# Optimization experiments

Measured on AMD Instinct MI355X. Metric: run time of the kernel, lower is better.

## Reference

```python
import jax, jax.numpy as jnp
import numpy as np

AUDIO_DIM, TEXT_DIM, HIDDEN_DIM = 512, 768, 512
B, AUDIO_LEN, TEXT_LEN = 8, 2048, 512


def setup_inputs() -> dict:
    key = jax.random.key(0)
    ks = jax.random.split(key, 9)
    audio_features = jax.random.normal(ks[0], (B, AUDIO_LEN, AUDIO_DIM), dtype=jnp.float32)
    text_features = jax.random.normal(ks[1], (B, TEXT_LEN, TEXT_DIM), dtype=jnp.float32)
    text_mask = jax.random.randint(ks[2], (B, TEXT_LEN), 0, 2).astype(jnp.int32)
    # Linear params (PyTorch default init scale ~ U(-1/sqrt(fan_in), 1/sqrt(fan_in)))
    def lin(kw, kb, fan_in, fan_out):
        bound = 1.0 / np.sqrt(fan_in)
        W = jax.random.uniform(kw, (fan_in, fan_out), minval=-bound, maxval=bound, dtype=jnp.float32)
        b = jax.random.uniform(kb, (fan_out,), minval=-bound, maxval=bound, dtype=jnp.float32)
        return W, b
    Wq, bq = lin(ks[3], ks[4], AUDIO_DIM, HIDDEN_DIM)
    Wk, bk = lin(ks[5], ks[6], TEXT_DIM, HIDDEN_DIM)
    Wv, bv = lin(ks[7], ks[8], TEXT_DIM, HIDDEN_DIM)
    return {
        "audio_features": audio_features,
        "text_features": text_features,
        "Wq": Wq, "bq": bq, "Wk": Wk, "bk": bk, "Wv": Wv, "bv": bv,
        "text_mask": text_mask,
    }


def reference(audio_features, text_features, Wq, bq, Wk, bk, Wv, bv, text_mask):
    scale = HIDDEN_DIM ** -0.5
    q = jnp.einsum("bad,dh->bah", audio_features, Wq) + bq  # (B, A, H)
    k = jnp.einsum("btd,dh->bth", text_features, Wk) + bk   # (B, T, H)
    v = jnp.einsum("btd,dh->bth", text_features, Wv) + bv   # (B, T, H)
    scores = jnp.einsum("bah,bth->bat", q, k) * scale        # (B, A, T)
    mask = text_mask[:, None, :]  # (B, 1, T)
    scores = jnp.where(mask == 0, -jnp.inf, scores)
    attn = jax.nn.softmax(scores, axis=-1)
    # dropout is identity in eval mode
    enhanced_audio = jnp.einsum("bat,bth->bah", attn, v)     # (B, A, H)
    return enhanced_audio
```

## Files before the change

kernel.cpp:

```cpp
#include <hip/hip_runtime.h>
#include <cstdint>
#include <cstddef>

#define AUDIO_DIM 512
#define TEXT_DIM  768
#define HIDDEN    512
#define BATCH     8
#define ALEN      2048
#define TLEN      512

typedef _Float16 half8 __attribute__((ext_vector_type(8)));
typedef _Float16 half4_t __attribute__((ext_vector_type(4)));
typedef float floatx4 __attribute__((ext_vector_type(4)));

#define AS1 __attribute__((address_space(1)))
#define AS3 __attribute__((address_space(3)))

__device__ __forceinline__ void gload_lds16(const void* g, void* l) {
    __builtin_amdgcn_global_load_lds((const AS1 void*)g, (AS3 void*)l, 16, 0, 0);
}

__device__ __forceinline__ int swz(int r) { return (r >> 1) & 3; }

__global__ __launch_bounds__(256) void prep(
    const float* __restrict__ audio, const float* __restrict__ text,
    const float* __restrict__ Wq, const float* __restrict__ Wk,
    const float* __restrict__ Wv,
    _Float16* __restrict__ audio_h, _Float16* __restrict__ text_h,
    _Float16* __restrict__ Wq_t, _Float16* __restrict__ Wk_t,
    _Float16* __restrict__ Wv_t)
{
    __shared__ _Float16 tt[32 * 33];
    const int bid = blockIdx.x, tid = threadIdx.x;
    if (bid < 11264) {
        const float* src; _Float16* dst; int i;
        if (bid < 8192) { src = audio; dst = audio_h; i = bid * 256 + tid; }
        else            { src = text;  dst = text_h;  i = (bid - 8192) * 256 + tid; }
        float4 v = ((const float4*)src)[i];
        half4_t h;
        h.x = (_Float16)v.x; h.y = (_Float16)v.y; h.z = (_Float16)v.z; h.w = (_Float16)v.w;
        ((half4_t*)dst)[i] = h;
    } else {
        const float* src; _Float16* dst; int R, lb;
        if (bid < 11520)      { lb = bid - 11264; src = Wq; dst = Wq_t; R = 512; }
        else if (bid < 11904) { lb = bid - 11520; src = Wk; dst = Wk_t; R = 768; }
        else                  { lb = bid - 11904; src = Wv; dst = Wv_t; R = 768; }
        const int C = 512;
        const int c0 = (lb & 15) * 32, r0 = (lb >> 4) * 32;
        const int tx = tid & 31, ty = tid >> 5;
#pragma unroll
        for (int i = 0; i < 4; i++) {
            int r = ty + i * 8;
            tt[r * 33 + tx] = (_Float16)src[(size_t)(r0 + r) * C + c0 + tx];
        }
        __syncthreads();
#pragma unroll
        for (int i = 0; i < 4; i++) {
            int r = ty + i * 8;
            dst[(size_t)(c0 + r) * R + r0 + tx] = tt[tx * 33 + r];
        }
    }
}

template <bool OUT16, bool ROWBIAS>
__device__ __forceinline__ void gemm_body(
    const _Float16* __restrict__ A, const _Float16* __restrict__ Bt,
    const float* __restrict__ bias, void* __restrict__ Cp,
    int N, int K, int m0, int n0, _Float16* Asm, _Float16* Bsm)
{
    const int tid = threadIdx.x;
    const int l = tid & 63, w = tid >> 6;
    const int wm = w >> 1, wn = w & 1;
    const int srow = l >> 2, sj = l & 3;
    const int q = l >> 4, c16 = l & 15;

    floatx4 acc[4][4] = {};

    for (int k0 = 0; k0 < K; k0 += 32) {
        if (k0) __syncthreads();
#pragma unroll
        for (int i = 0; i < 2; i++) {
            int rb = (w * 2 + i) * 16;
            int r = rb + srow;
            int cc = sj ^ swz(r);
            gload_lds16(A + (size_t)(m0 + r) * K + k0 + cc * 8, Asm + rb * 32);
            gload_lds16(Bt + (size_t)(n0 + r) * K + k0 + cc * 8, Bsm + rb * 32);
        }
        __syncthreads();

        half8 af[4], bf[4];
#pragma unroll
        for (int t = 0; t < 4; t++) {
            int rA = wm * 64 + t * 16 + c16;
            af[t] = *(const half8*)&Asm[rA * 32 + ((q ^ swz(rA)) << 3)];
            int rB = wn * 64 + t * 16 + c16;
            bf[t] = *(const half8*)&Bsm[rB * 32 + ((q ^ swz(rB)) << 3)];
        }
#pragma unroll
        for (int mi = 0; mi < 4; mi++)
#pragma unroll
            for (int ni = 0; ni < 4; ni++)
                acc[mi][ni] = __builtin_amdgcn_mfma_f32_16x16x32_f16(
                    af[mi], bf[ni], acc[mi][ni], 0, 0, 0);
    }

    if (OUT16) {
        float bcol[4];
        float brow[4][4];
        if (!ROWBIAS) {
#pragma unroll
            for (int ni = 0; ni < 4; ni++)
                bcol[ni] = bias[n0 + wn * 64 + ni * 16 + c16];
        } else {
#pragma unroll
            for (int mi = 0; mi < 4; mi++) {
                float4 b4 = *(const float4*)&bias[m0 + wm * 64 + mi * 16 + q * 4];
                brow[mi][0] = b4.x; brow[mi][1] = b4.y;
                brow[mi][2] = b4.z; brow[mi][3] = b4.w;
            }
        }
        _Float16* C = (_Float16*)Cp;
#pragma unroll
        for (int ni = 0; ni < 4; ni++) {
            int col = n0 + wn * 64 + ni * 16 + c16;
#pragma unroll
            for (int mi = 0; mi < 4; mi++) {
                int row = m0 + wm * 64 + mi * 16 + q * 4;
#pragma unroll
                for (int r = 0; r < 4; r++) {
                    float b = ROWBIAS ? brow[mi][r] : bcol[ni];
                    C[(size_t)(row + r) * N + col] = (_Float16)(acc[mi][ni][r] + b);
                }
            }
        }
    } else {
        float* C = (float*)Cp;
#pragma unroll
        for (int ni = 0; ni < 4; ni++) {
            int col = n0 + wn * 64 + ni * 16 + c16;
#pragma unroll
            for (int mi = 0; mi < 4; mi++) {
                int row = m0 + wm * 64 + mi * 16 + q * 4;
#pragma unroll
                for (int r = 0; r < 4; r++)
                    C[(size_t)(row + r) * N + col] = acc[mi][ni][r];
            }
        }
    }
}

__global__ __launch_bounds__(256, 2) void qkv_gemm(
    const _Float16* __restrict__ audio_h, const _Float16* __restrict__ text_h,
    const _Float16* __restrict__ Wq_t, const _Float16* __restrict__ Wk_t,
    const _Float16* __restrict__ Wv_t,
    const float* __restrict__ bq, const float* __restrict__ bk,
    const float* __restrict__ bv,
    _Float16* __restrict__ Qh, _Float16* __restrict__ Kh,
    _Float16* __restrict__ Vt)
{
    __shared__ __align__(16) _Float16 Asm[128 * 32];
    __shared__ __align__(16) _Float16 Bsm[128 * 32];
    const int bid = blockIdx.x;
    if (bid < 512) {
        gemm_body<true, false>(audio_h, Wq_t, bq, Qh, 512, 512,
                               (bid >> 2) * 128, (bid & 3) * 128, Asm, Bsm);
    } else if (bid < 640) {
        int lb = bid - 512;
        gemm_body<true, false>(text_h, Wk_t, bk, Kh, 512, 768,
                               (lb >> 2) * 128, (lb & 3) * 128, Asm, Bsm);
    } else {
        int lb = bid - 640;
        int z = lb >> 4, by = (lb >> 2) & 3, bx = lb & 3;
        gemm_body<true, true>(Wv_t, text_h + (size_t)z * 393216, bv,
                              Vt + (size_t)z * 262144, 512, 768,
                              by * 128, bx * 128, Asm, Bsm);
    }
}

#define QT 32
#define PSTR 544

__global__ __launch_bounds__(256, 2) void attn_fused(
    const _Float16* __restrict__ Qh, const _Float16* __restrict__ Kh,
    const _Float16* __restrict__ Vt, const int* __restrict__ mask,
    float* __restrict__ out)
{
    __shared__ __align__(16) _Float16 Qs[QT * 32];
    __shared__ __align__(16) _Float16 KV[512 * 32];
    __shared__ __align__(16) _Float16 Pl[QT * PSTR];
    __shared__ float red[4][QT];
    __shared__ float red2[4][QT];
    const int tid = threadIdx.x, l = tid & 63, w = tid >> 6;
    const int b = blockIdx.y, a0 = blockIdx.x * QT;
    const _Float16* Qb = Qh + (size_t)(b * ALEN + a0) * HIDDEN;
    const _Float16* Kb = Kh + (size_t)b * TLEN * HIDDEN;
    const _Float16* Vb = Vt + (size_t)b * HIDDEN * TLEN;
    const int srow = l >> 2, sj = l & 3;
    const int q = l >> 4, c16 = l & 15;

    floatx4 acc[2][8] = {};
    for (int k0 = 0; k0 < HIDDEN; k0 += 32) {
        if (k0) __syncthreads();
        if (w < 2) {
            int rb = w * 16;
            int r = rb + srow;
            int cc = sj ^ swz(r);
            gload_lds16(Qb + (size_t)r * HIDDEN + k0 + cc * 8, Qs + rb * 32);
        }
#pragma unroll
        for (int i = 0; i < 8; i++) {
            int rb = (w * 8 + i) * 16;
            int r = rb + srow;
            int cc = sj ^ swz(r);
            gload_lds16(Kb + (size_t)r * HIDDEN + k0 + cc * 8, KV + rb * 32);
        }
        __syncthreads();

        half8 af[2], bf[8];
#pragma unroll
        for (int t = 0; t < 2; t++) {
            int rA = t * 16 + c16;
            af[t] = *(const half8*)&Qs[rA * 32 + ((q ^ swz(rA)) << 3)];
        }
#pragma unroll
        for (int t = 0; t < 8; t++) {
            int rB = w * 128 + t * 16 + c16;
            bf[t] = *(const half8*)&KV[rB * 32 + ((q ^ swz(rB)) << 3)];
        }
#pragma unroll
        for (int mi = 0; mi < 2; mi++)
#pragma unroll
            for (int ni = 0; ni < 8; ni++)
                acc[mi][ni] = __builtin_amdgcn_mfma_f32_16x16x32_f16(
                    af[mi], bf[ni], acc[mi][ni], 0, 0, 0);
    }

    const float scale = 0.044194173824159216f;
    int mv[8];
#pragma unroll
    for (int ni = 0; ni < 8; ni++)
        mv[ni] = mask[b * TLEN + w * 128 + ni * 16 + c16];
#pragma unroll
    for (int mi = 0; mi < 2; mi++)
#pragma unroll
        for (int ni = 0; ni < 8; ni++)
#pragma unroll
            for (int r = 0; r < 4; r++)
                acc[mi][ni][r] = mv[ni] ? acc[mi][ni][r] * scale : -1e30f;

    float mx[2][4];
#pragma unroll
    for (int mi = 0; mi < 2; mi++)
#pragma unroll
        for (int r = 0; r < 4; r++) {
            float m = -1e30f;
#pragma unroll
            for (int ni = 0; ni < 8; ni++) m = fmaxf(m, acc[mi][ni][r]);
#pragma unroll
            for (int off = 1; off <= 8; off <<= 1) m = fmaxf(m, __shfl_xor(m, off));
            mx[mi][r] = m;
        }
    if (c16 == 0)
#pragma unroll
        for (int mi = 0; mi < 2; mi++)
#pragma unroll
            for (int r = 0; r < 4; r++) red[w][mi * 16 + q * 4 + r] = mx[mi][r];
    __syncthreads();
#pragma unroll
    for (int mi = 0; mi < 2; mi++)
#pragma unroll
        for (int r = 0; r < 4; r++) {
            int row = mi * 16 + q * 4 + r;
            mx[mi][r] = fmaxf(fmaxf(red[0][row], red[1][row]),
                              fmaxf(red[2][row], red[3][row]));
        }

    float sm[2][4];
#pragma unroll
    for (int mi = 0; mi < 2; mi++)
#pragma unroll
        for (int r = 0; r < 4; r++) {
            float s = 0.f;
#pragma unroll
            for (int ni = 0; ni < 8; ni++) {
                float e = __expf(acc[mi][ni][r] - mx[mi][r]);
                acc[mi][ni][r] = e;
                s += e;
            }
#pragma unroll
            for (int off = 1; off <= 8; off <<= 1) s += __shfl_xor(s, off);
            sm[mi][r] = s;
        }
    if (c16 == 0)
#pragma unroll
        for (int mi = 0; mi < 2; mi++)
#pragma unroll
            for (int r = 0; r < 4; r++) red2[w][mi * 16 + q * 4 + r] = sm[mi][r];
    __syncthreads();

#pragma unroll
    for (int mi = 0; mi < 2; mi++)
#pragma unroll
        for (int r = 0; r < 4; r++) {
            int row = mi * 16 + q * 4 + r;
            float inv = 1.f / (red2[0][row] + red2[1][row] + red2[2][row] + red2[3][row]);
#pragma unroll
            for (int ni = 0; ni < 8; ni++) {
                int t = w * 128 + ni * 16 + c16;
                int chunk = t >> 3;
                int chunkS = (chunk & ~3) | ((chunk & 3) ^ ((row >> 1) & 3));
                Pl[row * PSTR + chunkS * 8 + (t & 7)] = (_Float16)(acc[mi][ni][r] * inv);
            }
        }
    __syncthreads();

    floatx4 oacc[2][8] = {};
    for (int k0 = 0; k0 < TLEN; k0 += 32) {
        if (k0) __syncthreads();
#pragma unroll
        for (int i = 0; i < 8; i++) {
            int rb = (w * 8 + i) * 16;
            int r = rb + srow;
            int cc = sj ^ swz(r);
            gload_lds16(Vb + (size_t)r * TLEN + k0 + cc * 8, KV + rb * 32);
        }
        __syncthreads();

        half8 pf[2], vf[8];
#pragma unroll
        for (int mi = 0; mi < 2; mi++) {
            int row = mi * 16 + c16;
            int chunkS = (k0 >> 3) + (q ^ ((c16 >> 1) & 3));
            pf[mi] = *(const half8*)&Pl[row * PSTR + chunkS * 8];
        }
#pragma unroll
        for (int t = 0; t < 8; t++) {
            int rB = w * 128 + t * 16 + c16;
            vf[t] = *(const half8*)&KV[rB * 32 + ((q ^ swz(rB)) << 3)];
        }
#pragma unroll
        for (int mi = 0; mi < 2; mi++)
#pragma unroll
            for (int ni = 0; ni < 8; ni++)
                oacc[mi][ni] = __builtin_amdgcn_mfma_f32_16x16x32_f16(
                    pf[mi], vf[ni], oacc[mi][ni], 0, 0, 0);
    }

#pragma unroll
    for (int ni = 0; ni < 8; ni++) {
        int col = w * 128 + ni * 16 + c16;
#pragma unroll
        for (int mi = 0; mi < 2; mi++) {
            int row = mi * 16 + q * 4;
#pragma unroll
            for (int r = 0; r < 4; r++)
                out[(size_t)(b * ALEN + a0 + row + r) * HIDDEN + col] =
                    oacc[mi][ni][r];
        }
    }
}

extern "C" void kernel_launch(void* const* d_in, const int* in_sizes, int n_in,
                              void* d_out, int out_size, void* d_ws, size_t ws_size,
                              hipStream_t stream)
{
    const float* audio = (const float*)d_in[0];
    const float* text  = (const float*)d_in[1];
    const float* Wq    = (const float*)d_in[2];
    const float* bq    = (const float*)d_in[3];
    const float* Wk    = (const float*)d_in[4];
    const float* bk    = (const float*)d_in[5];
    const float* Wv    = (const float*)d_in[6];
    const float* bv    = (const float*)d_in[7];
    const int*   maskp = (const int*)d_in[8];
    float* out = (float*)d_out;

    _Float16* audio_h = (_Float16*)d_out;

    _Float16* ws16   = (_Float16*)d_ws;
    _Float16* text_h = ws16;
    _Float16* Wq_t   = text_h + 3145728;
    _Float16* Wk_t   = Wq_t + 262144;
    _Float16* Wv_t   = Wk_t + 393216;
    _Float16* Kh     = Wv_t + 393216;
    _Float16* Vt     = Kh + 2097152;
    _Float16* Qh     = Vt + 2097152;

    prep<<<12288, 256, 0, stream>>>(audio, text, Wq, Wk, Wv,
                                    audio_h, text_h, Wq_t, Wk_t, Wv_t);
    qkv_gemm<<<768, 256, 0, stream>>>(audio_h, text_h, Wq_t, Wk_t, Wv_t,
                                      bq, bk, bv, Qh, Kh, Vt);
    attn_fused<<<dim3(ALEN / QT, BATCH), 256, 0, stream>>>(Qh, Kh, Vt, maskp, out);
}
```

Baseline: 177.8 us.

## Load Q/K/V MFMA fragments directly from global memory, drop LDS staging

The attention kernel now reads Q, K and V operand fragments straight from global memory into registers rather than staging them through shared memory with global_load_lds and barriers. This removes the per-iteration __syncthreads and frees the Qs/KV LDS buffers, and the launch bound is raised to 4 blocks per CU for more occupancy. In exchange each wave issues strided 16-byte global loads, and there is no longer any sharing of K/V tiles within a block, so the design leans on L1/L2 caching. The higher occupancy target may also cause register spills given the large accumulator arrays.

Result: slower. 222.9 us (+25.4%).

```diff
diff --git a/kernel.cpp b/kernel.cpp
--- a/kernel.cpp
+++ b/kernel.cpp
@@ -180,13 +180,11 @@
 #define QT 32
 #define PSTR 544
 
-__global__ __launch_bounds__(256, 2) void attn_fused(
+__global__ __launch_bounds__(256, 4) void attn_fused(
     const _Float16* __restrict__ Qh, const _Float16* __restrict__ Kh,
     const _Float16* __restrict__ Vt, const int* __restrict__ mask,
     float* __restrict__ out)
 {
-    __shared__ __align__(16) _Float16 Qs[QT * 32];
-    __shared__ __align__(16) _Float16 KV[512 * 32];
     __shared__ __align__(16) _Float16 Pl[QT * PSTR];
     __shared__ float red[4][QT];
     __shared__ float red2[4][QT];
@@ -195,38 +193,27 @@
     const _Float16* Qb = Qh + (size_t)(b * ALEN + a0) * HIDDEN;
     const _Float16* Kb = Kh + (size_t)b * TLEN * HIDDEN;
     const _Float16* Vb = Vt + (size_t)b * HIDDEN * TLEN;
-    const int srow = l >> 2, sj = l & 3;
     const int q = l >> 4, c16 = l & 15;
 
+    const _Float16* arow[2];
+#pragma unroll
+    for (int mi = 0; mi < 2; mi++)
+        arow[mi] = Qb + (size_t)(mi * 16 + c16) * HIDDEN + q * 8;
+    const _Float16* brow[8];
+#pragma unroll
+    for (int ni = 0; ni < 8; ni++)
+        brow[ni] = Kb + (size_t)(w * 128 + ni * 16 + c16) * HIDDEN + q * 8;
+
     floatx4 acc[2][8] = {};
+#pragma unroll 4
     for (int k0 = 0; k0 < HIDDEN; k0 += 32) {
-        if (k0) __syncthreads();
-        if (w < 2) {
-            int rb = w * 16;
-            int r = rb + srow;
-            int cc = sj ^ swz(r);
-            gload_lds16(Qb + (size_t)r * HIDDEN + k0 + cc * 8, Qs + rb * 32);
-        }
-#pragma unroll
-        for (int i = 0; i < 8; i++) {
-            int rb = (w * 8 + i) * 16;
-            int r = rb + srow;
-            int cc = sj ^ swz(r);
-            gload_lds16(Kb + (size_t)r * HIDDEN + k0 + cc * 8, KV + rb * 32);
-        }
-        __syncthreads();
-
         half8 af[2], bf[8];
 #pragma unroll
-        for (int t = 0; t < 2; t++) {
-            int rA = t * 16 + c16;
-            af[t] = *(const half8*)&Qs[rA * 32 + ((q ^ swz(rA)) << 3)];
-        }
-#pragma unroll
-        for (int t = 0; t < 8; t++) {
-            int rB = w * 128 + t * 16 + c16;
-            bf[t] = *(const half8*)&KV[rB * 32 + ((q ^ swz(rB)) << 3)];
-        }
+        for (int mi = 0; mi < 2; mi++)
+            af[mi] = *(const half8*)(arow[mi] + k0);
+#pragma unroll
+        for (int ni = 0; ni < 8; ni++)
+            bf[ni] = *(const half8*)(brow[ni] + k0);
 #pragma unroll
         for (int mi = 0; mi < 2; mi++)
 #pragma unroll
@@ -314,18 +301,14 @@
         }
     __syncthreads();
 
+    const _Float16* vrow[8];
+#pragma unroll
+    for (int ni = 0; ni < 8; ni++)
+        vrow[ni] = Vb + (size_t)(w * 128 + ni * 16 + c16) * TLEN + q * 8;
+
     floatx4 oacc[2][8] = {};
+#pragma unroll 4
     for (int k0 = 0; k0 < TLEN; k0 += 32) {
-        if (k0) __syncthreads();
-#pragma unroll
-        for (int i = 0; i < 8; i++) {
-            int rb = (w * 8 + i) * 16;
-            int r = rb + srow;
-            int cc = sj ^ swz(r);
-            gload_lds16(Vb + (size_t)r * TLEN + k0 + cc * 8, KV + rb * 32);
-        }
-        __syncthreads();
-
         half8 pf[2], vf[8];
 #pragma unroll
         for (int mi = 0; mi < 2; mi++) {
@@ -334,10 +317,8 @@
             pf[mi] = *(const half8*)&Pl[row * PSTR + chunkS * 8];
         }
 #pragma unroll
-        for (int t = 0; t < 8; t++) {
-            int rB = w * 128 + t * 16 + c16;
-            vf[t] = *(const half8*)&KV[rB * 32 + ((q ^ swz(rB)) << 3)];
-        }
+        for (int ni = 0; ni < 8; ni++)
+            vf[ni] = *(const half8*)(vrow[ni] + k0);
 #pragma unroll
         for (int mi = 0; mi < 2; mi++)
 #pragma unroll
```

## Register-prefetch K/V tiles and load Q fragments directly from global

Applied to the files above, without the earlier changes.

Replaces the direct global-to-LDS loads in the attention kernel with register double-buffering. The next K or V tile is loaded into registers while MFMAs run on the current LDS tile, and Q fragments now come straight from global memory into registers, which removes the Qs shared buffer. __syncthreads is replaced by a custom barrier that waits only on lgkmcnt (LDS and scalar counters), so the barrier does not stall on outstanding vector memory loads. This hides global-load latency at the cost of many more VGPRs, which may cut occupancy under launch_bounds(256,2) or cause spills.

Result: no change. 179.4 us (+0.9%).

```diff
diff --git a/kernel.cpp b/kernel.cpp
--- a/kernel.cpp
+++ b/kernel.cpp
@@ -21,6 +21,10 @@
 }
 
 __device__ __forceinline__ int swz(int r) { return (r >> 1) & 3; }
+
+__device__ __forceinline__ void wg_barrier_lds() {
+    asm volatile("s_waitcnt lgkmcnt(0)\n\ts_barrier" ::: "memory");
+}
 
 __global__ __launch_bounds__(256) void prep(
     const float* __restrict__ audio, const float* __restrict__ text,
@@ -185,7 +189,6 @@
     const _Float16* __restrict__ Vt, const int* __restrict__ mask,
     float* __restrict__ out)
 {
-    __shared__ __align__(16) _Float16 Qs[QT * 32];
     __shared__ __align__(16) _Float16 KV[512 * 32];
     __shared__ __align__(16) _Float16 Pl[QT * PSTR];
     __shared__ float red[4][QT];
@@ -198,30 +201,45 @@
     const int srow = l >> 2, sj = l & 3;
     const int q = l >> 4, c16 = l & 15;
 
+    const _Float16* arow[2];
+#pragma unroll
+    for (int mi = 0; mi < 2; mi++)
+        arow[mi] = Qb + (size_t)(mi * 16 + c16) * HIDDEN + q * 8;
+
+    half8 kvr[8], kvn[8];
+    half8 af[2], afn[2];
+#pragma unroll
+    for (int i = 0; i < 8; i++) {
+        int rb = (w * 8 + i) * 16;
+        int r = rb + srow;
+        int cc = sj ^ swz(r);
+        kvr[i] = *(const half8*)(Kb + (size_t)r * HIDDEN + cc * 8);
+    }
+#pragma unroll
+    for (int mi = 0; mi < 2; mi++) af[mi] = *(const half8*)(arow[mi]);
+
     floatx4 acc[2][8] = {};
-    for (int k0 = 0; k0 < HIDDEN; k0 += 32) {
-        if (k0) __syncthreads();
-        if (w < 2) {
-            int rb = w * 16;
-            int r = rb + srow;
-            int cc = sj ^ swz(r);
-            gload_lds16(Qb + (size_t)r * HIDDEN + k0 + cc * 8, Qs + rb * 32);
-        }
+    for (int it = 0; it < 16; ++it) {
 #pragma unroll
         for (int i = 0; i < 8; i++) {
             int rb = (w * 8 + i) * 16;
-            int r = rb + srow;
-            int cc = sj ^ swz(r);
-            gload_lds16(Kb + (size_t)r * HIDDEN + k0 + cc * 8, KV + rb * 32);
-        }
-        __syncthreads();
-
-        half8 af[2], bf[8];
-#pragma unroll
-        for (int t = 0; t < 2; t++) {
-            int rA = t * 16 + c16;
-            af[t] = *(const half8*)&Qs[rA * 32 + ((q ^ swz(rA)) << 3)];
-        }
+            *(half8*)&KV[rb * 32 + l * 8] = kvr[i];
+        }
+        wg_barrier_lds();
+        if (it < 15) {
+            int k1 = (it + 1) * 32;
+#pragma unroll
+            for (int i = 0; i < 8; i++) {
+                int rb = (w * 8 + i) * 16;
+                int r = rb + srow;
+                int cc = sj ^ swz(r);
+                kvn[i] = *(const half8*)(Kb + (size_t)r * HIDDEN + k1 + cc * 8);
+            }
+#pragma unroll
+            for (int mi = 0; mi < 2; mi++)
+                afn[mi] = *(const half8*)(arow[mi] + k1);
+        }
+        half8 bf[8];
 #pragma unroll
         for (int t = 0; t < 8; t++) {
             int rB = w * 128 + t * 16 + c16;
@@ -233,6 +251,11 @@
             for (int ni = 0; ni < 8; ni++)
                 acc[mi][ni] = __builtin_amdgcn_mfma_f32_16x16x32_f16(
                     af[mi], bf[ni], acc[mi][ni], 0, 0, 0);
+        wg_barrier_lds();
+#pragma unroll
+        for (int i = 0; i < 8; i++) kvr[i] = kvn[i];
+#pragma unroll
+        for (int mi = 0; mi < 2; mi++) af[mi] = afn[mi];
     }
 
     const float scale = 0.044194173824159216f;
@@ -265,7 +288,7 @@
         for (int mi = 0; mi < 2; mi++)
 #pragma unroll
             for (int r = 0; r < 4; r++) red[w][mi * 16 + q * 4 + r] = mx[mi][r];
-    __syncthreads();
+    wg_barrier_lds();
 #pragma unroll
     for (int mi = 0; mi < 2; mi++)
 #pragma unroll
@@ -296,7 +319,7 @@
         for (int mi = 0; mi < 2; mi++)
 #pragma unroll
             for (int r = 0; r < 4; r++) red2[w][mi * 16 + q * 4 + r] = sm[mi][r];
-    __syncthreads();
+    wg_barrier_lds();
 
 #pragma unroll
     for (int mi = 0; mi < 2; mi++)
@@ -312,20 +335,35 @@
                 Pl[row * PSTR + chunkS * 8 + (t & 7)] = (_Float16)(acc[mi][ni][r] * inv);
             }
         }
-    __syncthreads();
+    wg_barrier_lds();
+
+#pragma unroll
+    for (int i = 0; i < 8; i++) {
+        int rb = (w * 8 + i) * 16;
+        int r = rb + srow;
+        int cc = sj ^ swz(r);
+        kvr[i] = *(const half8*)(Vb + (size_t)r * TLEN + cc * 8);
+    }
 
     floatx4 oacc[2][8] = {};
-    for (int k0 = 0; k0 < TLEN; k0 += 32) {
-        if (k0) __syncthreads();
+    for (int it = 0; it < 16; ++it) {
+        int k0 = it * 32;
 #pragma unroll
         for (int i = 0; i < 8; i++) {
             int rb = (w * 8 + i) * 16;
-            int r = rb + srow;
-            int cc = sj ^ swz(r);
-            gload_lds16(Vb + (size_t)r * TLEN + k0 + cc * 8, KV + rb * 32);
-        }
-        __syncthreads();
-
+            *(half8*)&KV[rb * 32 + l * 8] = kvr[i];
+        }
+        wg_barrier_lds();
+        if (it < 15) {
+            int k1 = k0 + 32;
+#pragma unroll
+            for (int i = 0; i < 8; i++) {
+                int rb = (w * 8 + i) * 16;
+                int r = rb + srow;
+                int cc = sj ^ swz(r);
+                kvn[i] = *(const half8*)(Vb + (size_t)r * TLEN + k1 + cc * 8);
+            }
+        }
         half8 pf[2], vf[8];
 #pragma unroll
         for (int mi = 0; mi < 2; mi++) {
@@ -344,6 +382,9 @@
             for (int ni = 0; ni < 8; ni++)
                 oacc[mi][ni] = __builtin_amdgcn_mfma_f32_16x16x32_f16(
                     pf[mi], vf[ni], oacc[mi][ni], 0, 0, 0);
+        wg_barrier_lds();
+#pragma unroll
+        for (int i = 0; i < 8; i++) kvr[i] = kvn[i];
     }
 
 #pragma unroll
```
